# Kernel tuning notes

Hardware: AMD Instinct MI355X
Metric: run time of the kernel (lower is better)

Reference implementation:

```python
import jax, jax.numpy as jnp
import numpy as np

WS = 8   # window_size
SS = 4   # shift_size = window_size // 2
HEADS = 8
DH = 16  # dim_head


def _rel_index(ws):
    c = np.arange(ws)
    coords = np.stack(np.meshgrid(c, c, indexing='ij')).reshape(2, -1)  # [2, ws*ws]
    rel = (coords[:, :, None] - coords[:, None, :]).transpose(1, 2, 0)  # [l, l, 2]
    rel[..., 0] += ws - 1
    rel[..., 1] += ws - 1
    rel[..., 0] *= 2 * ws - 1
    return rel.sum(-1)  # [l, l] int


def _make_mask(H, W, ws, ss):
    img = np.zeros((H, W), np.float32)
    sl = (slice(0, -ws), slice(-ws, -ss), slice(-ss, None))
    cnt = 0
    for hs in sl:
        for wcs in sl:
            img[hs, wcs] = cnt
            cnt += 1
    win = img.reshape(H // ws, ws, W // ws, ws).transpose(0, 2, 1, 3).reshape(-1, ws * ws)
    diff = win[:, None, :] - win[:, :, None]  # [nW, l, l]
    return np.where(diff != 0, -np.inf, 0.0).astype(np.float32)


def _ln(x, g, b, eps=1e-5):
    m = x.mean(-1, keepdims=True)
    v = ((x - m) ** 2).mean(-1, keepdims=True)
    return (x - m) * jax.lax.rsqrt(v + eps) * g + b


def _part(t, ws):
    B, H, W, C = t.shape
    return t.reshape(B, H // ws, ws, W // ws, ws, C).transpose(0, 1, 3, 2, 4, 5).reshape(-1, ws * ws, C)


def _unpart(t, ws, B, H, W):
    C = t.shape[-1]
    return t.reshape(B, H // ws, W // ws, ws, ws, C).transpose(0, 1, 3, 2, 4, 5).reshape(B, H, W, C)


def _block(x, illu, p, shift, mask, ridx):
    B, H, W, C = x.shape
    ws = WS
    l = ws * ws
    g1, b1, qw, qb, tbl, pw, pb, g2, b2, f1w, f1b, f2w, f2b = p
    shortcut = x
    xn = _ln(x, g1, b1)
    if shift > 0:
        xn = jnp.roll(xn, (-shift, -shift), (1, 2))
        illu = jnp.roll(illu, (-shift, -shift), (1, 2))
    xw = _part(xn, ws)     # [n, l, C]
    iw = _part(illu, ws)   # [n, l, C]
    n = xw.shape[0]
    qkv = (xw @ qw + qb).reshape(n, l, 3, HEADS, DH).transpose(2, 0, 3, 1, 4)
    q, k, v = qkv[0], qkv[1], qkv[2]  # each [n, h, l, d]
    attn = jnp.einsum('nhld,nhmd->nhlm', q * (DH ** -0.5), k)
    bias = tbl[ridx].transpose(2, 0, 1)  # [h, l, l]
    attn = attn + bias[None]
    # illumination modulation of V
    v = v * iw.reshape(n, l, HEADS, DH).transpose(0, 2, 1, 3)
    if mask is not None:
        nw = mask.shape[0]
        attn = (attn.reshape(B, nw, HEADS, l, l) + mask[None, :, None]).reshape(n, HEADS, l, l)
    attn = jax.nn.softmax(attn, axis=-1)
    out = jnp.einsum('nhlm,nhmd->nhld', attn, v).transpose(0, 2, 1, 3).reshape(n, l, C)
    out = out @ pw + pb
    out = _unpart(out, ws, B, H, W)
    if shift > 0:
        out = jnp.roll(out, (shift, shift), (1, 2))
    x = shortcut + out
    y = _ln(x, g2, b2)
    y = jax.nn.gelu(y @ f1w + f1b, approximate=False) @ f2w + f2b
    return x + y


def setup_inputs() -> dict:
    key = jax.random.key(0)
    ks = jax.random.split(key, 8)
    B, C, H, W = 4, 128, 256, 256
    NB, HID, TBL = 2, 512, 225
    r = lambda k, s, sc=1.0: jax.random.normal(k, s, jnp.float32) * sc
    return {
        'x': r(ks[0], (B, C, H, W)),
        'illu_fea': r(ks[1], (B, C, H, W)),
        'norm1_g': jnp.ones((NB, C), jnp.float32),
        'norm1_b': jnp.zeros((NB, C), jnp.float32),
        'qkv_w': r(ks[2], (NB, C, 3 * C), 0.02),
        'qkv_b': jnp.zeros((NB, 3 * C), jnp.float32),
        'bias_table': r(ks[3], (NB, TBL, HEADS), 0.02),
        'proj_w': r(ks[4], (NB, C, C), 0.02),
        'proj_b': jnp.zeros((NB, C), jnp.float32),
        'norm2_g': jnp.ones((NB, C), jnp.float32),
        'norm2_b': jnp.zeros((NB, C), jnp.float32),
        'fc1_w': r(ks[5], (NB, C, HID), 0.02),
        'fc1_b': jnp.zeros((NB, HID), jnp.float32),
        'fc2_w': r(ks[6], (NB, HID, C), 0.02),
        'fc2_b': jnp.zeros((NB, C), jnp.float32),
    }


def reference(x, illu_fea, norm1_g, norm1_b, qkv_w, qkv_b, bias_table, proj_w, proj_b, norm2_g, norm2_b, fc1_w, fc1_b, fc2_w, fc2_b):
    B, C, H, W = x.shape
    xb = x.transpose(0, 2, 3, 1)
    ib = illu_fea.transpose(0, 2, 3, 1)
    ridx = _rel_index(WS)
    mask = jnp.asarray(_make_mask(H, W, WS, SS))
    nb = norm1_g.shape[0]
    for i in range(nb):
        shift = 0 if i % 2 == 0 else SS
        p = (norm1_g[i], norm1_b[i], qkv_w[i], qkv_b[i], bias_table[i], proj_w[i], proj_b[i],
             norm2_g[i], norm2_b[i], fc1_w[i], fc1_b[i], fc2_w[i], fc2_b[i])
        xb = _block(xb, ib, p, shift, mask if shift > 0 else None, ridx)
    return xb.transpose(0, 3, 1, 2)
```

## Files before the change

kernel.cpp:

```cpp
#include <hip/hip_runtime.h>
#include <hip/hip_bf16.h>

typedef unsigned short u16;
typedef __attribute__((ext_vector_type(8))) short bfrag;
typedef __attribute__((ext_vector_type(4))) float f32x4;
typedef __attribute__((ext_vector_type(2))) int i32x2;
typedef __attribute__((ext_vector_type(4))) int i32x4;

constexpr int OFF_N1G  = 64;
constexpr int OFF_N1B  = OFF_N1G + 256;
constexpr int OFF_QKVB = OFF_N1B + 256;
constexpr int OFF_PB   = OFF_QKVB + 768;
constexpr int OFF_N2G  = OFF_PB + 256;
constexpr int OFF_N2B  = OFF_N2G + 256;
constexpr int OFF_F1B  = OFF_N2B + 256;
constexpr int OFF_F2B  = OFF_F1B + 1024;
constexpr int OFF_BIAS = OFF_F2B + 256;
constexpr int OFF_QWT  = OFF_BIAS + 65536;
constexpr int OFF_PWT  = OFF_QWT + 49152;
constexpr int OFF_F1WT = OFF_PWT + 16384;
constexpr int OFF_F2WT = OFF_F1WT + 65536;
constexpr long OFF_XBUF = 265728;
constexpr long OFF_IBUF = OFF_XBUF + 33554432;

__device__ __forceinline__ float blo(unsigned w) { return __uint_as_float(w << 16); }
__device__ __forceinline__ u16 f2b(float f) {
  unsigned u = __float_as_uint(f);
  u += 0x7fffu + ((u >> 16) & 1u);
  return (u16)(u >> 16);
}
__device__ __forceinline__ unsigned f2b_pk(float a, float b) {
  unsigned r;
  asm("v_cvt_pk_bf16_f32 %0, %1, %2" : "=v"(r) : "v"(a), "v"(b));
  return r;
}
__device__ __forceinline__ float ldin(const void* p, long i, int bf) {
  if (bf) return blo((unsigned)((const u16*)p)[i]);
  return ((const float*)p)[i];
}
__device__ __forceinline__ f32x4 mfma16(bfrag a, bfrag b, f32x4 c) {
  return __builtin_amdgcn_mfma_f32_16x16x32_bf16(a, b, c, 0, 0, 0);
}
__device__ __forceinline__ float fast_gelu(float x) {
  const float z = fabsf(x) * 0.70710678118f;
  const float tt = __builtin_amdgcn_rcpf(1.0f + 0.3275911f * z);
  const float poly = tt * (0.254829592f + tt * (-0.284496736f + tt * (1.421413741f +
                     tt * (-1.453152027f + tt * 1.061405429f))));
  const float erfz = 1.0f - poly * __expf(-z * z);
  return x * 0.5f * (1.0f + copysignf(erfz, x));
}

__global__ void k_sniff(const u16* __restrict__ x, int* __restrict__ flag) {
  __shared__ int sc[4];
  const int t = threadIdx.x;
  int c = 0;
  for (int i = t; i < 4096; i += 256) {
    const int e = (x[2 * i] >> 7) & 0xFF;
    c += (e >= 96 && e <= 143) ? 1 : 0;
  }
  #pragma unroll
  for (int o = 32; o; o >>= 1) c += __shfl_down(c, o);
  if ((t & 63) == 0) sc[t >> 6] = c;
  __syncthreads();
  if (t == 0) *flag = ((sc[0] + sc[1] + sc[2] + sc[3]) > 2400) ? 1 : 0;
}

__global__ void k_convert(const void* __restrict__ src, float* __restrict__ dst, int n,
                          const int* __restrict__ flagp) {
  const int bf = *flagp;
  const int i = blockIdx.x * 256 + threadIdx.x;
  if (i < n) dst[i] = ldin(src, i, bf);
}

__global__ void k_cvtT(const void* __restrict__ src, u16* __restrict__ dst, int K, int N,
                       const int* __restrict__ flagp) {
  const int bf = *flagp;
  const int id = blockIdx.x * 256 + threadIdx.x;
  const int KN = K * N;
  if (id >= 2 * KN) return;
  const int l = id / KN, r = id % KN;
  const int n = r % N, k = r / N;
  const float v = ldin(src, (long)l * KN + (long)k * N + n, bf);
  dst[((long)l * N + n) * K + k] = f2b(v);
}

__global__ void k_cvtF1(const void* __restrict__ src, u16* __restrict__ dst,
                        const int* __restrict__ flagp) {
  const int bf = *flagp;
  const int id = blockIdx.x * 256 + threadIdx.x;
  const int l = id >> 16, r = id & 65535;
  const int k = r >> 9, n = r & 511;
  const float v = ldin(src, (long)l * 65536 + k * 512 + n, bf);
  dst[(long)l * 65536 + (n >> 6) * 8192 + (((n & 63) * 128 + k) ^ ((n & 7) << 3))] = f2b(v);
}
__global__ void k_cvtF2(const void* __restrict__ src, u16* __restrict__ dst,
                        const int* __restrict__ flagp) {
  const int bf = *flagp;
  const int id = blockIdx.x * 256 + threadIdx.x;
  const int l = id >> 16, r = id & 65535;
  const int k = r >> 7, n = r & 127;
  const float v = ldin(src, (long)l * 65536 + k * 128 + n, bf);
  dst[(long)l * 65536 + (k >> 6) * 8192 + ((n * 64 + (k & 63)) ^ ((n & 7) << 3))] = f2b(v);
}

__global__ void k_bias(const void* __restrict__ tbl, float* __restrict__ dst,
                       const int* __restrict__ flagp) {
  const int bf = *flagp;
  const int id = blockIdx.x * 256 + threadIdx.x;
  const int j = id & 63, i = (id >> 6) & 63;
  const int idx = ((i >> 3) - (j >> 3) + 7) * 15 + ((i & 7) - (j & 7) + 7);
  const int h = (id >> 12) & 7, l = id >> 15;
  dst[(id & ~4095) + j * 64 + i] = ldin(tbl, (long)l * 1800 + idx * 8 + h, bf);
}

__global__ __launch_bounds__(256) void k_tin(const void* __restrict__ src,
                                             const void* __restrict__ il,
                                             float* __restrict__ dst,
                                             u16* __restrict__ idst,
                                             const int* __restrict__ flagp) {
  __shared__ float tile[64][65];
  const int bf = *flagp;
  const int bid = blockIdx.x;
  const int cb = bid & 1, wb = (bid >> 1) & 3, h = (bid >> 3) & 255, b = bid >> 11;
  const int tw = threadIdx.x & 63, tg = threadIdx.x >> 6;
  #pragma unroll
  for (int i = 0; i < 16; ++i) {
    const int c = i * 4 + tg;
    tile[c][tw] = ldin(src, ((long)((b * 128 + cb * 64 + c) * 256 + h)) * 256 + wb * 64 + tw, bf);
  }
  __syncthreads();
  #pragma unroll
  for (int i = 0; i < 16; ++i) {
    const int wl = i * 4 + tg;
    const int pix = (b * 256 + h) * 256 + wb * 64 + wl;
    dst[(size_t)pix * 128 + cb * 64 + tw] = tile[tw][wl];
  }
  __syncthreads();
  #pragma unroll
  for (int i = 0; i < 16; ++i) {
    const int c = i * 4 + tg;
    tile[c][tw] = ldin(il, ((long)((b * 128 + cb * 64 + c) * 256 + h)) * 256 + wb * 64 + tw, bf);
  }
  __syncthreads();
  #pragma unroll
  for (int i = 0; i < 16; ++i) {
    const int wl = i * 4 + tg;
    const int pix = (b * 256 + h) * 256 + wb * 64 + wl;
    idst[(size_t)pix * 128 + cb * 64 + tw] = f2b(tile[tw][wl]);
  }
}

__device__ __forceinline__ int xn_addr(int tok, int chunk) {
  return tok * 128 + ((chunk ^ (tok & 7)) << 3);
}

__global__ __launch_bounds__(512, 4) void k_attnP(
    float* xbuf, const u16* __restrict__ ibuf,
    const float* __restrict__ wsf,
    const u16* __restrict__ qwT, const u16* __restrict__ pwT,
    const float* __restrict__ biasb, const int blk, const int shift)
{
  __shared__ __align__(16) u16 smem[32768];
  u16* xn = smem;
  u16* Q2 = smem + 8192;
  u16* K2 = smem + 16384;
  u16* VT = smem + 24576;
  u16* O  = smem + 24576;

  const int t = threadIdx.x, l = t & 63, w = t >> 6;
  const int win = blockIdx.x;
  const int b = win >> 10, wh = (win >> 5) & 31, wn = win & 31;
  const int g = l >> 4, c16 = l & 15, c8 = c16 * 8;

  const float* g1 = wsf + OFF_N1G + blk * 128;
  const float* b1 = wsf + OFF_N1B + blk * 128;
  const float* qb = wsf + OFF_QKVB + blk * 384;
  const u16* qwl = qwT + (size_t)blk * 49152;

  float iw[4][4];
  {
    const u16* ip = ibuf + (size_t)b * 8388608 + w * 16 + c16;
    #pragma unroll
    for (int rt = 0; rt < 4; ++rt)
      #pragma unroll
      for (int r = 0; r < 4; ++r) {
        const int tok = rt * 16 + g * 4 + r;
        const int hh = (wh * 8 + (tok >> 3) + shift) & 255;
        const int wp = (wn * 8 + (tok & 7) + shift) & 255;
        iw[rt][r] = blo(ip[(size_t)((hh << 8) + wp) * 128]);
      }
  }

  {
    float gg[8], bb[8];
    *(float4*)&gg[0] = *(const float4*)(g1 + c8);
    *(float4*)&gg[4] = *(const float4*)(g1 + c8 + 4);
    *(float4*)&bb[0] = *(const float4*)(b1 + c8);
    *(float4*)&bb[4] = *(const float4*)(b1 + c8 + 4);
    #pragma unroll
    for (int s = 0; s < 2; ++s) {
      const int tok = w * 8 + s * 4 + g;
      const int hh = (wh * 8 + (tok >> 3) + shift) & 255;
      const int wp = (wn * 8 + (tok & 7) + shift) & 255;
      const float* xr = xbuf + (size_t)((b * 256 + hh) * 256 + wp) * 128 + c8;
      float v[8];
      *(float4*)&v[0] = *(const float4*)xr;
      *(float4*)&v[4] = *(const float4*)(xr + 4);
      float sm = 0.f, sq = 0.f;
      #pragma unroll
      for (int j = 0; j < 8; ++j) { sm += v[j]; sq = fmaf(v[j], v[j], sq); }
      #pragma unroll
      for (int o = 8; o; o >>= 1) { sm += __shfl_xor(sm, o); sq += __shfl_xor(sq, o); }
      const float mean = sm * 0.0078125f;
      const float rstd = rsqrtf(fmaf(-mean, mean, sq * 0.0078125f) + 1e-5f);
      unsigned pk[4];
      #pragma unroll
      for (int jj = 0; jj < 4; ++jj) {
        const float o0 = (v[2 * jj] - mean) * rstd * gg[2 * jj] + bb[2 * jj];
        const float o1 = (v[2 * jj + 1] - mean) * rstd * gg[2 * jj + 1] + bb[2 * jj + 1];
        pk[jj] = f2b_pk(o0, o1);
      }
      i32x4 st; st[0] = (int)pk[0]; st[1] = (int)pk[1]; st[2] = (int)pk[2]; st[3] = (int)pk[3];
      *(i32x4*)&xn[(tok * 128 + c8) ^ ((tok & 7) << 3)] = st;
    }
  }
  __syncthreads();

  {
    const int colv = (16 + w) * 16 + c16;
    const float bv = qb[colv];
    f32x4 acv[4];
    #pragma unroll
    for (int rt = 0; rt < 4; ++rt) acv[rt] = (f32x4){bv, bv, bv, bv};
    const u16* bp = qwl + colv * 128 + g * 8;
    #pragma unroll
    for (int kt = 0; kt < 4; ++kt) {
      const bfrag bw = *(const bfrag*)(bp + kt * 32);
      #pragma unroll
      for (int rt = 0; rt < 4; ++rt) {
        const bfrag a = *(const bfrag*)&xn[xn_addr(rt * 16 + c16, kt * 4 + g)];
        acv[rt] = mfma16(a, bw, acv[rt]);
      }
    }
    u16* vt = VT + w * 1024 + c16 * 64;
    const int sx = (c16 & 7) << 3;
    #pragma unroll
    for (int rt = 0; rt < 4; ++rt) {
      const unsigned p0 = f2b_pk(acv[rt][0] * iw[rt][0], acv[rt][1] * iw[rt][1]);
      const unsigned p1 = f2b_pk(acv[rt][2] * iw[rt][2], acv[rt][3] * iw[rt][3]);
      i32x2 pp; pp[0] = (int)p0; pp[1] = (int)p1;
      *(i32x2*)&vt[(rt * 16 + g * 4) ^ sx] = pp;
    }
  }

  {
    const int colq = w * 16 + c16;
    const float bq = qb[colq];
    f32x4 acq[4];
    #pragma unroll
    for (int rt = 0; rt < 4; ++rt) acq[rt] = (f32x4){bq, bq, bq, bq};
    const u16* bpq = qwl + colq * 128 + g * 8;
    #pragma unroll
    for (int kt = 0; kt < 4; ++kt) {
      const bfrag bwq = *(const bfrag*)(bpq + kt * 32);
      #pragma unroll
      for (int rt = 0; rt < 4; ++rt) {
        const bfrag a = *(const bfrag*)&xn[xn_addr(rt * 16 + c16, kt * 4 + g)];
        acq[rt] = mfma16(a, bwq, acq[rt]);
      }
    }
    u16* dq = Q2 + w * 1024 + ((c16 >> 3) * 64) * 8 + (c16 & 7);
    #pragma unroll
    for (int rt = 0; rt < 4; ++rt)
      #pragma unroll
      for (int r = 0; r < 4; ++r)
        dq[(rt * 16 + g * 4 + r) * 8] = f2b(acq[rt][r]);
  }
  {
    const int colk = 128 + w * 16 + c16;
    const float bk = qb[colk];
    f32x4 ack[4];
    #pragma unroll
    for (int rt = 0; rt < 4; ++rt) ack[rt] = (f32x4){bk, bk, bk, bk};
    const u16* bpk = qwl + colk * 128 + g * 8;
    #pragma unroll
    for (int kt = 0; kt < 4; ++kt) {
      const bfrag bwk = *(const bfrag*)(bpk + kt * 32);
      #pragma unroll
      for (int rt = 0; rt < 4; ++rt) {
        const bfrag a = *(const bfrag*)&xn[xn_addr(rt * 16 + c16, kt * 4 + g)];
        ack[rt] = mfma16(a, bwk, ack[rt]);
      }
    }
    u16* dk = K2 + w * 1024 + ((c16 >> 3) * 64) * 8 + (c16 & 7);
    #pragma unroll
    for (int rt = 0; rt < 4; ++rt)
      #pragma unroll
      for (int r = 0; r < 4; ++r)
        dk[(rt * 16 + g * 4 + r) * 8] = f2b(ack[rt][r]);
  }

  const bfrag zfrag = {0, 0, 0, 0, 0, 0, 0, 0};
  const f32x4 zacc = {0.f, 0.f, 0.f, 0.f};
  bfrag kf[4];
  #pragma unroll
  for (int jt = 0; jt < 4; ++jt) {
    bfrag v = zfrag;
    if (l < 32) v = *(const bfrag*)&K2[w * 1024 + (g * 64 + jt * 16 + c16) * 8];
    kf[jt] = v;
  }
  bfrag vb[2];
  {
    const int sx = (c16 & 7) << 3;
    #pragma unroll
    for (int kt = 0; kt < 2; ++kt)
      vb[kt] = *(const bfrag*)&VT[w * 1024 + c16 * 64 + ((kt * 32 + g * 8) ^ sx)];
  }
  __syncthreads();

  const float* bl2 = biasb + blk * 32768 + w * 4096;
  const bool mk = (shift > 0) && ((wh == 31) || (wn == 31));
  int lj[4];
  if (mk) {
    #pragma unroll
    for (int jt = 0; jt < 4; ++jt) {
      const int j = jt * 16 + c16;
      lj[jt] = ((wh == 31) ? (((j >> 3) < 4) ? 1 : 2) : 0) * 3 +
               ((wn == 31) ? (((j & 7) < 4) ? 1 : 2) : 0);
    }
  }
  u16* Pw = K2 + w * 1024;

  #pragma unroll
  for (int it = 0; it < 4; ++it) {
    bfrag qf = zfrag;
    if (l < 32) qf = *(const bfrag*)&Q2[w * 1024 + (g * 64 + it * 16 + c16) * 8];
    f32x4 s4[4];
    #pragma unroll
    for (int jt = 0; jt < 4; ++jt) s4[jt] = mfma16(qf, kf[jt], zacc);

    #pragma unroll
    for (int jt = 0; jt < 4; ++jt) {
      const float4 bv4 = *(const float4*)&bl2[(jt * 16 + c16) * 64 + it * 16 + g * 4];
      #pragma unroll
      for (int r = 0; r < 4; ++r)
        s4[jt][r] = fmaf(s4[jt][r], 0.25f, (&bv4.x)[r]);
    }
    if (mk) {
      #pragma unroll
      for (int r = 0; r < 4; ++r) {
        const int i = it * 16 + g * 4 + r;
        const int li = ((wh == 31) ? (((i >> 3) < 4) ? 1 : 2) : 0) * 3 +
                       ((wn == 31) ? (((i & 7) < 4) ? 1 : 2) : 0);
        #pragma unroll
        for (int jt = 0; jt < 4; ++jt)
          if (li != lj[jt]) s4[jt][r] = -1e30f;
      }
    }

    #pragma unroll
    for (int r = 0; r < 4; ++r) {
      float mx = fmaxf(fmaxf(s4[0][r], s4[1][r]), fmaxf(s4[2][r], s4[3][r]));
      #pragma unroll
      for (int o = 8; o; o >>= 1) mx = fmaxf(mx, __shfl_xor(mx, o));
      float e0 = __expf(s4[0][r] - mx);
      float e1 = __expf(s4[1][r] - mx);
      float e2 = __expf(s4[2][r] - mx);
      float e3 = __expf(s4[3][r] - mx);
      float sm = e0 + e1 + e2 + e3;
      #pragma unroll
      for (int o = 8; o; o >>= 1) sm += __shfl_xor(sm, o);
      const float inv = 1.0f / sm;
      s4[0][r] = e0 * inv; s4[1][r] = e1 * inv;
      s4[2][r] = e2 * inv; s4[3][r] = e3 * inv;
    }

    #pragma unroll
    for (int jt = 0; jt < 4; ++jt)
      #pragma unroll
      for (int r = 0; r < 4; ++r)
        Pw[(g * 4 + r) * 40 + jt * 16 + c16] = f2b(s4[jt][r]);
    const bfrag pa0 = *(const bfrag*)&Pw[c16 * 40 + g * 8];
    const bfrag pa1 = *(const bfrag*)&Pw[c16 * 40 + 32 + g * 8];
    f32x4 o = zacc;
    o = mfma16(pa0, vb[0], o);
    o = mfma16(pa1, vb[1], o);
    #pragma unroll
    for (int r = 0; r < 4; ++r) {
      const int tok = it * 16 + g * 4 + r;
      O[tok * 128 + (((w * 2 + (c16 >> 3)) ^ (tok & 7)) << 3) + (c16 & 7)] = f2b(o[r]);
    }
  }
  __syncthreads();

  {
    const int prt = w & 3, ph = w >> 2;
    bfrag af[4];
    #pragma unroll
    for (int kt = 0; kt < 4; ++kt)
      af[kt] = *(const bfrag*)&O[xn_addr(prt * 16 + c16, kt * 4 + g)];
    const u16* pwl = pwT + blk * 16384;
    const float* pb = wsf + OFF_PB + blk * 128;
    #pragma unroll
    for (int ct = 0; ct < 4; ++ct) {
      const int col = ph * 64 + ct * 16 + c16;
      const float bv = pb[col];
      f32x4 ac = {bv, bv, bv, bv};
      const u16* bp = pwl + col * 128 + g * 8;
      #pragma unroll
      for (int kt = 0; kt < 4; ++kt) ac = mfma16(af[kt], *(const bfrag*)(bp + kt * 32), ac);
      #pragma unroll
      for (int r = 0; r < 4; ++r) {
        const int tok = prt * 16 + g * 4 + r;
        const int hh = (wh * 8 + (tok >> 3) + shift) & 255;
        const int wp = (wn * 8 + (tok & 7) + shift) & 255;
        const size_t xi = (size_t)((b * 256 + hh) * 256 + wp) * 128 + col;
        xbuf[xi] += ac[r];
      }
    }
  }
}

__global__ __launch_bounds__(256, 3) void k_ffn(
    float* xbuf, const float* __restrict__ wsf,
    const u16* __restrict__ f1S, const u16* __restrict__ f2S,
    const int blk, void* __restrict__ outp, const int last,
    const int* __restrict__ flagp)
{
  __shared__ __align__(16) u16 B0[8192];
  __shared__ __align__(16) u16 B1[8192];
  __shared__ __align__(16) u16 hid[8192];
  __shared__ float sbias[512];
  const int bfl = *flagp;
  const int t = threadIdx.x, l = t & 63, w = t >> 6;
  u16* hw = hid + w * 2048;
  const int pix0 = blockIdx.x * 64;
  const float* g2 = wsf + OFF_N2G + blk * 128;
  const float* b2 = wsf + OFF_N2B + blk * 128;
  const float* f1bp = wsf + OFF_F1B + blk * 512;
  const float* f2bp = wsf + OFF_F2B + blk * 128;
  const u16* f1 = f1S + (size_t)blk * 65536;
  const u16* f2 = f2S + (size_t)blk * 65536;

  auto STAGE = [&](const u16* src, u16* dstbuf) {
    const u16* gp = src + w * 2048 + l * 8;
    u16* d = dstbuf + w * 2048;
    #pragma unroll
    for (int q = 0; q < 4; ++q)
      __builtin_amdgcn_global_load_lds(gp + q * 512, d + q * 512, 16, 0, 0);
  };
  auto tsrc = [&](int i) -> const u16* {
    const int cc = i >> 2, pp = i & 3;
    return (pp < 2 ? f1 : f2) + cc * 16384 + (pp & 1) * 8192;
  };

  STAGE(tsrc(0), B0);
  sbias[t] = f1bp[t];
  sbias[t + 256] = f1bp[t + 256];

  {
    const int g = l >> 4, c16 = l & 15, c8 = c16 * 8;
    float gg[8], bb[8];
    *(float4*)&gg[0] = *(const float4*)(g2 + c8);
    *(float4*)&gg[4] = *(const float4*)(g2 + c8 + 4);
    *(float4*)&bb[0] = *(const float4*)(b2 + c8);
    *(float4*)&bb[4] = *(const float4*)(b2 + c8 + 4);
    #pragma unroll
    for (int s = 0; s < 4; ++s) {
      const int tt = s * 4 + g;
      const float* xr = xbuf + (size_t)(pix0 + w * 16 + tt) * 128 + c8;
      float v[8];
      *(float4*)&v[0] = *(const float4*)xr;
      *(float4*)&v[4] = *(const float4*)(xr + 4);
      float sm = 0.f, sq = 0.f;
      #pragma unroll
      for (int j = 0; j < 8; ++j) { sm += v[j]; sq = fmaf(v[j], v[j], sq); }
      #pragma unroll
      for (int o = 8; o; o >>= 1) { sm += __shfl_xor(sm, o); sq += __shfl_xor(sq, o); }
      const float mean = sm * 0.0078125f;
      const float rstd = rsqrtf(fmaf(-mean, mean, sq * 0.0078125f) + 1e-5f);
      unsigned pk[4];
      #pragma unroll
      for (int jj = 0; jj < 4; ++jj) {
        const float o0 = (v[2 * jj] - mean) * rstd * gg[2 * jj] + bb[2 * jj];
        const float o1 = (v[2 * jj + 1] - mean) * rstd * gg[2 * jj + 1] + bb[2 * jj + 1];
        pk[jj] = f2b_pk(o0, o1);
      }
      i32x4 st; st[0] = (int)pk[0]; st[1] = (int)pk[1]; st[2] = (int)pk[2]; st[3] = (int)pk[3];
      *(i32x4*)&hw[(tt * 128 + c8) ^ ((tt & 7) << 3)] = st;
    }
  }
  bfrag af[4];
  #pragma unroll
  for (int kt = 0; kt < 4; ++kt)
    af[kt] = *(const bfrag*)&hw[((l & 15) * 128 + kt * 32 + (l >> 4) * 8) ^ (((l & 15) & 7) << 3)];

  f32x4 y[8];
  #pragma unroll
  for (int ct = 0; ct < 8; ++ct) {
    const float bv = f2bp[ct * 16 + (l & 15)];
    y[ct] = (f32x4){bv, bv, bv, bv};
  }

  for (int c = 0; c < 4; ++c) {
    #pragma unroll
    for (int p = 0; p < 4; ++p) {
      const int i = c * 4 + p;
      if (i < 15) STAGE(tsrc(i + 1), (i & 1) ? B0 : B1);
      if (i == 0) asm volatile("s_waitcnt vmcnt(4) lgkmcnt(0)" ::: "memory");
      else if (i < 15) asm volatile("s_waitcnt vmcnt(4)" ::: "memory");
      else asm volatile("s_waitcnt vmcnt(0)" ::: "memory");
      __builtin_amdgcn_sched_barrier(0);
      __builtin_amdgcn_s_barrier();
      const u16* BUF = (i & 1) ? B1 : B0;
      if (p < 2) {
        #pragma unroll
        for (int c1 = 0; c1 < 4; ++c1) {
          const int wcol = c1 * 16 + (l & 15);
          const int n = p * 64 + wcol;
          const float bv = sbias[c * 128 + n];
          f32x4 a1 = {bv, bv, bv, bv};
          #pragma unroll
          for (int kt = 0; kt < 4; ++kt) {
            const bfrag bw = *(const bfrag*)&BUF[(wcol * 128 + kt * 32 + (l >> 4) * 8) ^ ((wcol & 7) << 3)];
            a1 = mfma16(af[kt], bw, a1);
          }
          #pragma unroll
          for (int r = 0; r < 4; ++r) {
            const int row = (l >> 4) * 4 + r;
            hw[(row * 128 + n) ^ ((row & 7) << 3)] = f2b(fast_gelu(a1[r]));
          }
        }
      } else {
        const int kh = p - 2;
        bfrag a2[2];
        #pragma unroll
        for (int kt = 0; kt < 2; ++kt)
          a2[kt] = *(const bfrag*)&hw[((l & 15) * 128 + kh * 64 + kt * 32 + (l >> 4) * 8) ^ (((l & 15) & 7) << 3)];
        #pragma unroll
        for (int ct = 0; ct < 8; ++ct) {
          const int col = ct * 16 + (l & 15);
          #pragma unroll
          for (int kt = 0; kt < 2; ++kt) {
            const bfrag bw = *(const bfrag*)&BUF[(col * 64 + kt * 32 + (l >> 4) * 8) ^ ((col & 7) << 3)];
            y[ct] = mfma16(a2[kt], bw, y[ct]);
          }
        }
      }
      __builtin_amdgcn_s_barrier();
    }
  }

  #pragma unroll
  for (int ct = 0; ct < 8; ++ct)
    #pragma unroll
    for (int r = 0; r < 4; ++r) {
      const int tok = w * 16 + (l >> 4) * 4 + r;
      const int pix = pix0 + tok;
      const int col = ct * 16 + (l & 15);
      const float rv = xbuf[(size_t)pix * 128 + col] + y[ct][r];
      if (last) {
        const int wp = pix & 255, hh2 = (pix >> 8) & 255, bb = pix >> 16;
        const long oi = (((long)bb * 128 + col) * 256 + hh2) * 256 + wp;
        if (bfl) ((u16*)outp)[oi] = f2b(rv);
        else ((float*)outp)[oi] = rv;
      } else {
        xbuf[(size_t)pix * 128 + col] = rv;
      }
    }
}

extern "C" void kernel_launch(void* const* d_in, const int* in_sizes, int n_in,
                              void* d_out, int out_size, void* d_ws, size_t ws_size,
                              hipStream_t stream) {
  (void)in_sizes; (void)n_in; (void)out_size; (void)ws_size;
  float* wsf = (float*)d_ws;
  int* flag = (int*)d_ws;
  const void* x = d_in[0];
  const void* illu = d_in[1];

  k_sniff<<<1, 256, 0, stream>>>((const u16*)x, flag);

  static const int cv_idx[8] = {2, 3, 5, 8, 9, 10, 12, 14};
  static const int cv_off[8] = {OFF_N1G, OFF_N1B, OFF_QKVB, OFF_PB, OFF_N2G, OFF_N2B, OFF_F1B, OFF_F2B};
  static const int cv_n[8] = {256, 256, 768, 256, 256, 256, 1024, 256};
  for (int i = 0; i < 8; ++i)
    k_convert<<<(cv_n[i] + 255) / 256, 256, 0, stream>>>(d_in[cv_idx[i]], wsf + cv_off[i], cv_n[i], flag);

  u16* qwT = (u16*)(wsf + OFF_QWT);
  u16* pwT = (u16*)(wsf + OFF_PWT);
  u16* f1wS = (u16*)(wsf + OFF_F1WT);
  u16* f2wS = (u16*)(wsf + OFF_F2WT);
  k_cvtT<<<384, 256, 0, stream>>>(d_in[4], qwT, 128, 384, flag);
  k_cvtT<<<128, 256, 0, stream>>>(d_in[7], pwT, 128, 128, flag);
  k_cvtF1<<<512, 256, 0, stream>>>(d_in[11], f1wS, flag);
  k_cvtF2<<<512, 256, 0, stream>>>(d_in[13], f2wS, flag);
  k_bias<<<256, 256, 0, stream>>>(d_in[6], wsf + OFF_BIAS, flag);

  float* xbuf = wsf + OFF_XBUF;
  u16* ibuf = (u16*)(wsf + OFF_IBUF);
  k_tin<<<8192, 256, 0, stream>>>(x, illu, xbuf, ibuf, flag);

  for (int blk = 0; blk < 2; ++blk) {
    const int shift = blk ? 4 : 0;
    k_attnP<<<4096, 512, 0, stream>>>(xbuf, ibuf, wsf, qwT, pwT, wsf + OFF_BIAS, blk, shift);
    k_ffn<<<4096, 256, 0, stream>>>(xbuf, wsf, f1wS, f2wS, blk, d_out, blk == 1 ? 1 : 0, flag);
  }
}
```

Baseline: 983.8 us.

## Fuse Q/K/V projection loops and change MLP hidden LDS swizzle

Merges the three separate Q, K and V projection GEMM loops into one loop, so each A fragment read from LDS feeds three MFMAs instead of being reloaded three times. The V-fragment readback is moved inside the fused block. A new XOR swizzle that also mixes row bits 3+ is applied to the MLP hidden buffer, meant to reduce LDS bank conflicts on the scalar GELU stores. The fused loop holds 12 accumulators at once, which raises register pressure and may lower occupancy.

```diff
diff --git a/kernel.cpp b/kernel.cpp
--- a/kernel.cpp
+++ b/kernel.cpp
@@ -41,6 +41,9 @@
 __device__ __forceinline__ f32x4 mfma16(bfrag a, bfrag b, f32x4 c) {
   return __builtin_amdgcn_mfma_f32_16x16x32_bf16(a, b, c, 0, 0, 0);
 }
+__device__ __forceinline__ int swr(int row) {
+  return ((row & 7) ^ ((row >> 3) << 1)) << 3;
+}
 __device__ __forceinline__ float fast_gelu(float x) {
   const float z = fabsf(x) * 0.70710678118f;
   const float tt = __builtin_amdgcn_rcpf(1.0f + 0.3275911f * z);
@@ -226,78 +229,58 @@
   }
   __syncthreads();
 
-  {
-    const int colv = (16 + w) * 16 + c16;
-    const float bv = qb[colv];
-    f32x4 acv[4];
-    #pragma unroll
-    for (int rt = 0; rt < 4; ++rt) acv[rt] = (f32x4){bv, bv, bv, bv};
-    const u16* bp = qwl + colv * 128 + g * 8;
-    #pragma unroll
-    for (int kt = 0; kt < 4; ++kt) {
-      const bfrag bw = *(const bfrag*)(bp + kt * 32);
-      #pragma unroll
-      for (int rt = 0; rt < 4; ++rt) {
-        const bfrag a = *(const bfrag*)&xn[xn_addr(rt * 16 + c16, kt * 4 + g)];
-        acv[rt] = mfma16(a, bw, acv[rt]);
-      }
-    }
-    u16* vt = VT + w * 1024 + c16 * 64;
-    const int sx = (c16 & 7) << 3;
-    #pragma unroll
-    for (int rt = 0; rt < 4; ++rt) {
-      const unsigned p0 = f2b_pk(acv[rt][0] * iw[rt][0], acv[rt][1] * iw[rt][1]);
-      const unsigned p1 = f2b_pk(acv[rt][2] * iw[rt][2], acv[rt][3] * iw[rt][3]);
-      i32x2 pp; pp[0] = (int)p0; pp[1] = (int)p1;
-      *(i32x2*)&vt[(rt * 16 + g * 4) ^ sx] = pp;
-    }
-  }
-
+  bfrag vb[2];
   {
     const int colq = w * 16 + c16;
-    const float bq = qb[colq];
-    f32x4 acq[4];
-    #pragma unroll
-    for (int rt = 0; rt < 4; ++rt) acq[rt] = (f32x4){bq, bq, bq, bq};
+    const int colk = colq + 128, colv = colq + 256;
+    const float bq = qb[colq], bk = qb[colk], bv = qb[colv];
+    f32x4 acq[4], ack[4], acv[4];
+    #pragma unroll
+    for (int rt = 0; rt < 4; ++rt) {
+      acq[rt] = (f32x4){bq, bq, bq, bq};
+      ack[rt] = (f32x4){bk, bk, bk, bk};
+      acv[rt] = (f32x4){bv, bv, bv, bv};
+    }
     const u16* bpq = qwl + colq * 128 + g * 8;
+    const u16* bpk = qwl + colk * 128 + g * 8;
+    const u16* bpv = qwl + colv * 128 + g * 8;
     #pragma unroll
     for (int kt = 0; kt < 4; ++kt) {
       const bfrag bwq = *(const bfrag*)(bpq + kt * 32);
+      const bfrag bwk = *(const bfrag*)(bpk + kt * 32);
+      const bfrag bwv = *(const bfrag*)(bpv + kt * 32);
       #pragma unroll
       for (int rt = 0; rt < 4; ++rt) {
         const bfrag a = *(const bfrag*)&xn[xn_addr(rt * 16 + c16, kt * 4 + g)];
         acq[rt] = mfma16(a, bwq, acq[rt]);
-      }
+        ack[rt] = mfma16(a, bwk, ack[rt]);
+        acv[rt] = mfma16(a, bwv, acv[rt]);
+      }
+    }
+    {
+      u16* vt = VT + w * 1024 + c16 * 64;
+      const int sx = (c16 & 7) << 3;
+      #pragma unroll
+      for (int rt = 0; rt < 4; ++rt) {
+        const unsigned p0 = f2b_pk(acv[rt][0] * iw[rt][0], acv[rt][1] * iw[rt][1]);
+        const unsigned p1 = f2b_pk(acv[rt][2] * iw[rt][2], acv[rt][3] * iw[rt][3]);
+        i32x2 pp; pp[0] = (int)p0; pp[1] = (int)p1;
+        *(i32x2*)&vt[(rt * 16 + g * 4) ^ sx] = pp;
+      }
+      #pragma unroll
+      for (int kt = 0; kt < 2; ++kt)
+        vb[kt] = *(const bfrag*)&VT[w * 1024 + c16 * 64 + ((kt * 32 + g * 8) ^ sx)];
     }
     u16* dq = Q2 + w * 1024 + ((c16 >> 3) * 64) * 8 + (c16 & 7);
+    u16* dk = K2 + w * 1024 + ((c16 >> 3) * 64) * 8 + (c16 & 7);
     #pragma unroll
     for (int rt = 0; rt < 4; ++rt)
       #pragma unroll
-      for (int r = 0; r < 4; ++r)
-        dq[(rt * 16 + g * 4 + r) * 8] = f2b(acq[rt][r]);
-  }
-  {
-    const int colk = 128 + w * 16 + c16;
-    const float bk = qb[colk];
-    f32x4 ack[4];
-    #pragma unroll
-    for (int rt = 0; rt < 4; ++rt) ack[rt] = (f32x4){bk, bk, bk, bk};
-    const u16* bpk = qwl + colk * 128 + g * 8;
-    #pragma unroll
-    for (int kt = 0; kt < 4; ++kt) {
-      const bfrag bwk = *(const bfrag*)(bpk + kt * 32);
-      #pragma unroll
-      for (int rt = 0; rt < 4; ++rt) {
-        const bfrag a = *(const bfrag*)&xn[xn_addr(rt * 16 + c16, kt * 4 + g)];
-        ack[rt] = mfma16(a, bwk, ack[rt]);
-      }
-    }
-    u16* dk = K2 + w * 1024 + ((c16 >> 3) * 64) * 8 + (c16 & 7);
-    #pragma unroll
-    for (int rt = 0; rt < 4; ++rt)
-      #pragma unroll
-      for (int r = 0; r < 4; ++r)
-        dk[(rt * 16 + g * 4 + r) * 8] = f2b(ack[rt][r]);
+      for (int r = 0; r < 4; ++r) {
+        const int tok = rt * 16 + g * 4 + r;
+        dq[tok * 8] = f2b(acq[rt][r]);
+        dk[tok * 8] = f2b(ack[rt][r]);
+      }
   }
 
   const bfrag zfrag = {0, 0, 0, 0, 0, 0, 0, 0};
@@ -308,13 +291,6 @@
     bfrag v = zfrag;
     if (l < 32) v = *(const bfrag*)&K2[w * 1024 + (g * 64 + jt * 16 + c16) * 8];
     kf[jt] = v;
-  }
-  bfrag vb[2];
-  {
-    const int sx = (c16 & 7) << 3;
-    #pragma unroll
-    for (int kt = 0; kt < 2; ++kt)
-      vb[kt] = *(const bfrag*)&VT[w * 1024 + c16 * 64 + ((kt * 32 + g * 8) ^ sx)];
   }
   __syncthreads();
 
@@ -487,13 +463,13 @@
         pk[jj] = f2b_pk(o0, o1);
       }
       i32x4 st; st[0] = (int)pk[0]; st[1] = (int)pk[1]; st[2] = (int)pk[2]; st[3] = (int)pk[3];
-      *(i32x4*)&hw[(tt * 128 + c8) ^ ((tt & 7) << 3)] = st;
+      *(i32x4*)&hw[(tt * 128 + c8) ^ swr(tt)] = st;
     }
   }
   bfrag af[4];
   #pragma unroll
   for (int kt = 0; kt < 4; ++kt)
-    af[kt] = *(const bfrag*)&hw[((l & 15) * 128 + kt * 32 + (l >> 4) * 8) ^ (((l & 15) & 7) << 3)];
+    af[kt] = *(const bfrag*)&hw[((l & 15) * 128 + kt * 32 + (l >> 4) * 8) ^ swr(l & 15)];
 
   f32x4 y[8];
   #pragma unroll
@@ -528,7 +504,7 @@
           #pragma unroll
           for (int r = 0; r < 4; ++r) {
             const int row = (l >> 4) * 4 + r;
-            hw[(row * 128 + n) ^ ((row & 7) << 3)] = f2b(fast_gelu(a1[r]));
+            hw[(row * 128 + n) ^ swr(row)] = f2b(fast_gelu(a1[r]));
           }
         }
       } else {
@@ -536,7 +512,7 @@
         bfrag a2[2];
         #pragma unroll
         for (int kt = 0; kt < 2; ++kt)
-          a2[kt] = *(const bfrag*)&hw[((l & 15) * 128 + kh * 64 + kt * 32 + (l >> 4) * 8) ^ (((l & 15) & 7) << 3)];
+          a2[kt] = *(const bfrag*)&hw[((l & 15) * 128 + kh * 64 + kt * 32 + (l >> 4) * 8) ^ swr(l & 15)];
         #pragma unroll
         for (int ct = 0; ct < 8; ++ct) {
           const int col = ct * 16 + (l & 15);
```

After: 980.0 us. About the same (-0.4%).
